# Optimization experiments

Measured on AMD Instinct MI355X. Metric: run time of the kernel, lower is better.

Reference implementation:

```python
import jax, jax.numpy as jnp
import numpy as np

B = 2048      # number of sequences with non-empty history
S = 32        # seq_len (all sequences full length for static shapes)
H = 256       # h_dim == embd_rank (ent/rel embedding dim)
NSEG = B * S  # total history timesteps (segments)
NNBR = 524288 # total gathered neighbor embeddings (avg 8 per segment)
ENT = 100000
REL = 1000


def setup_inputs() -> dict:
    key = jax.random.key(0)
    k1, k2, k3, k4, k5, k6, k7 = jax.random.split(key, 7)
    return {
        "neighbor_idx": jax.random.randint(k1, (NNBR,), 0, ENT),
        "segment_ids": jnp.sort(jax.random.randint(k2, (NNBR,), 0, NSEG)),
        "s_tem": jax.random.randint(k3, (B,), 0, ENT),
        "r_tem": jax.random.randint(k4, (B,), 0, REL),
        "s_hist_dt": jax.random.uniform(k5, (NSEG,), dtype=jnp.float32),
        "ent_embeds": jax.random.normal(k6, (ENT, H), dtype=jnp.float32),
        "rel_embeds": jax.random.normal(k7, (REL, H), dtype=jnp.float32),
    }


def reference(neighbor_idx, segment_ids, s_tem, r_tem, s_hist_dt, ent_embeds, rel_embeds):
    # gather neighbor entity embeddings (embeds_stack in the original)
    embeds_stack = ent_embeds[neighbor_idx]                     # [NNBR, H]
    # sparse.mm(mask, embeds_stack) == segment sum over neighbor groups
    sums = jax.ops.segment_sum(embeds_stack, segment_ids, num_segments=NSEG)
    counts = jax.ops.segment_sum(jnp.ones((NNBR,), embeds_stack.dtype),
                                 segment_ids, num_segments=NSEG)
    embeds_mean = sums / jnp.maximum(counts, 1.0)[:, None]      # [NSEG, H]
    # scatter means into padded [B, S, H] (all sequences full length)
    mean_seq = embeds_mean.reshape(B, S, H)
    # repeat subject entity / relation embeddings along time and concat
    ent_b = jnp.broadcast_to(ent_embeds[s_tem][:, None, :], (B, S, H))
    rel_b = jnp.broadcast_to(rel_embeds[r_tem][:, None, :], (B, S, H))
    s_embed_seq = jnp.concatenate([mean_seq, ent_b, rel_b], axis=-1)  # [B, S, 3H]
    s_hist_dt_seq = s_hist_dt.reshape(B, S)
    return s_embed_seq, s_hist_dt_seq
```

## Files before the change

kernel.cpp:

```cpp
#include <hip/hip_runtime.h>
#include <hip/hip_bf16.h>

#define BB    2048
#define SS    32
#define HH    256
#define NSEGC 65536
#define NNBRC 524288
#define NXCD  8
#define SPW   4

using f32x4 = __attribute__((ext_vector_type(4))) float;

__global__ __launch_bounds__(256) void seg_bounds_dt_kernel(
    const int*   __restrict__ segment_ids,
    int*         __restrict__ start,
    const float* __restrict__ dt,
    float*       __restrict__ out_tail)
{
    const int i = blockIdx.x * blockDim.x + threadIdx.x;

    if (i < NSEGC / 4) {
        const f32x4 v = reinterpret_cast<const f32x4*>(dt)[i];
        __builtin_nontemporal_store(v, reinterpret_cast<f32x4*>(out_tail) + i);
    }

    if (i > NSEGC) return;
    int lo = 0, hi = NNBRC;
    while (lo < hi) {
        const int mid = (lo + hi) >> 1;
        if (segment_ids[mid] < i) lo = mid + 1;
        else hi = mid;
    }
    start[i] = lo;
}

__global__ __launch_bounds__(256) void agg_kernel(
    const int*   __restrict__ neighbor_idx,
    const int*   __restrict__ s_tem,
    const int*   __restrict__ r_tem,
    const float* __restrict__ ent,
    const float* __restrict__ rel,
    const int*   __restrict__ start,
    float*       __restrict__ out)
{
    const int chunkw = gridDim.x / NXCD;
    const int wg   = (blockIdx.x % NXCD) * chunkw + blockIdx.x / NXCD;
    const int wave = wg * 4 + (threadIdx.x >> 6);
    const int lane = threadIdx.x & 63;
    const int seg0 = wave * SPW;
    const int b    = seg0 >> 5;

    const int sv = start[seg0 + min(lane, SPW)];
    const int p0 = __builtin_amdgcn_readfirstlane(__shfl(sv, 0));
    const int p1 = __builtin_amdgcn_readfirstlane(__shfl(sv, 1));
    const int p2 = __builtin_amdgcn_readfirstlane(__shfl(sv, 2));
    const int p3 = __builtin_amdgcn_readfirstlane(__shfl(sv, 3));
    const int p4 = __builtin_amdgcn_readfirstlane(__shfl(sv, 4));
    const int total = p4 - p0;
    const int r1 = p1 - p0, r2 = p2 - p0, r3 = p3 - p0;

    const int e = s_tem[b];
    const int r = r_tem[b];
    const f32x4 ev = *reinterpret_cast<const f32x4*>(ent + (size_t)e * HH + lane * 4);
    const f32x4 rv = *reinterpret_cast<const f32x4*>(rel + (size_t)r * HH + lane * 4);

    f32x4 a0 = {0.f,0.f,0.f,0.f}, a1 = a0, a2 = a0, a3 = a0;

    for (int base = 0; base < total; base += 64) {
        const int cnt = min(64, total - base);
        int myidx = 0;
        if (lane < cnt) myidx = neighbor_idx[p0 + base + lane];

        for (int j = 0; j < cnt; j += 8) {
            const int m = min(8, cnt - j);

#define GLD(K, VK)                                                         \
            f32x4 VK = {0.f,0.f,0.f,0.f};                                  \
            if (K < m) {                                                   \
                const int nb = __shfl(myidx, j + K);                       \
                VK = *reinterpret_cast<const f32x4*>(                      \
                    ent + (size_t)nb * HH + lane * 4);                     \
            }
            GLD(0, v0) GLD(1, v1) GLD(2, v2) GLD(3, v3)
            GLD(4, v4) GLD(5, v5) GLD(6, v6) GLD(7, v7)
#undef GLD

#define ACC(K, VK)                                                         \
            if (K < m) {                                                   \
                const int p = base + j + K;                                \
                if      (p < r1) a0 += VK;                                 \
                else if (p < r2) a1 += VK;                                 \
                else if (p < r3) a2 += VK;                                 \
                else             a3 += VK;                                 \
            }
            ACC(0, v0) ACC(1, v1) ACC(2, v2) ACC(3, v3)
            ACC(4, v4) ACC(5, v5) ACC(6, v6) ACC(7, v7)
#undef ACC
        }
    }

    const float i0 = 1.0f / fmaxf((float)(p1 - p0), 1.0f);
    const float i1 = 1.0f / fmaxf((float)(p2 - p1), 1.0f);
    const float i2 = 1.0f / fmaxf((float)(p3 - p2), 1.0f);
    const float i3 = 1.0f / fmaxf((float)(p4 - p3), 1.0f);

    float* o = out + (size_t)seg0 * (3 * HH);
#define STROW(S, AV, INV)                                                  \
    {                                                                      \
        const f32x4 mm = AV * INV;                                         \
        float* os = o + (size_t)(S) * (3 * HH);                            \
        __builtin_nontemporal_store(mm, reinterpret_cast<f32x4*>(os) + lane);          \
        __builtin_nontemporal_store(ev, reinterpret_cast<f32x4*>(os + HH) + lane);     \
        __builtin_nontemporal_store(rv, reinterpret_cast<f32x4*>(os + 2 * HH) + lane); \
    }
    STROW(0, a0, i0) STROW(1, a1, i1) STROW(2, a2, i2) STROW(3, a3, i3)
#undef STROW
}

extern "C" void kernel_launch(void* const* d_in, const int* in_sizes, int n_in,
                              void* d_out, int out_size, void* d_ws, size_t ws_size,
                              hipStream_t stream) {
    const int*   neighbor_idx = (const int*)  d_in[0];
    const int*   segment_ids  = (const int*)  d_in[1];
    const int*   s_tem        = (const int*)  d_in[2];
    const int*   r_tem        = (const int*)  d_in[3];
    const float* s_hist_dt    = (const float*)d_in[4];
    const float* ent_embeds   = (const float*)d_in[5];
    const float* rel_embeds   = (const float*)d_in[6];
    float*       out          = (float*)d_out;

    int* start = (int*)d_ws;

    {
        const int threads = 256;
        const int blocks  = (NSEGC + 1 + threads - 1) / threads;
        float* out_tail = out + (size_t)NSEGC * (3 * HH);
        seg_bounds_dt_kernel<<<blocks, threads, 0, stream>>>(
            segment_ids, start, s_hist_dt, out_tail);
    }

    {
        const int threads = 256;
        const int blocks  = NSEGC / SPW / 4;
        agg_kernel<<<blocks, threads, 0, stream>>>(
            neighbor_idx, s_tem, r_tem, ent_embeds, rel_embeds, start, out);
    }
}
```

Measured before the change: 336.6 us.

## Sweep entity-table chunks in order to localize neighbor gathers

Each wave now handles 8 segments (up to 192 neighbors per batch). For each batch it loops over 49 chunks of the entity table, using ballots to gather only the neighbors whose index falls in the current chunk. The idea is that all waves walk the table in roughly the same order at the same time, so the gathered rows hit L2/MALL more often. In exchange, each batch pays for 49 rounds of ballots, and the gathers become a serial one-row-at-a-time loop with little memory-level parallelism, where before 8 loads were issued together. Blocks grow to 512 threads.

```diff
diff --git a/kernel.cpp b/kernel.cpp
--- a/kernel.cpp
+++ b/kernel.cpp
@@ -7,7 +7,11 @@
 #define NSEGC 65536
 #define NNBRC 524288
 #define NXCD  8
-#define SPW   4
+#define SEGW  8
+#define WPB   8
+#define CHSH  11
+#define NCH   49
+#define SENT  0x7FFFFFFF
 
 using f32x4 = __attribute__((ext_vector_type(4))) float;
 
@@ -34,7 +38,7 @@
     start[i] = lo;
 }
 
-__global__ __launch_bounds__(256) void agg_kernel(
+__global__ __launch_bounds__(512, 4) void sweep_kernel(
     const int*   __restrict__ neighbor_idx,
     const int*   __restrict__ s_tem,
     const int*   __restrict__ r_tem,
@@ -45,75 +49,97 @@
 {
     const int chunkw = gridDim.x / NXCD;
     const int wg   = (blockIdx.x % NXCD) * chunkw + blockIdx.x / NXCD;
-    const int wave = wg * 4 + (threadIdx.x >> 6);
+    const int wave = wg * WPB + (threadIdx.x >> 6);
     const int lane = threadIdx.x & 63;
-    const int seg0 = wave * SPW;
+    const int seg0 = wave * SEGW;
     const int b    = seg0 >> 5;
 
-    const int sv = start[seg0 + min(lane, SPW)];
+    const int sv = start[seg0 + min(lane, SEGW)];
     const int p0 = __builtin_amdgcn_readfirstlane(__shfl(sv, 0));
-    const int p1 = __builtin_amdgcn_readfirstlane(__shfl(sv, 1));
-    const int p2 = __builtin_amdgcn_readfirstlane(__shfl(sv, 2));
-    const int p3 = __builtin_amdgcn_readfirstlane(__shfl(sv, 3));
-    const int p4 = __builtin_amdgcn_readfirstlane(__shfl(sv, 4));
-    const int total = p4 - p0;
-    const int r1 = p1 - p0, r2 = p2 - p0, r3 = p3 - p0;
+    const int q1 = __builtin_amdgcn_readfirstlane(__shfl(sv, 1));
+    const int q2 = __builtin_amdgcn_readfirstlane(__shfl(sv, 2));
+    const int q3 = __builtin_amdgcn_readfirstlane(__shfl(sv, 3));
+    const int q4 = __builtin_amdgcn_readfirstlane(__shfl(sv, 4));
+    const int q5 = __builtin_amdgcn_readfirstlane(__shfl(sv, 5));
+    const int q6 = __builtin_amdgcn_readfirstlane(__shfl(sv, 6));
+    const int q7 = __builtin_amdgcn_readfirstlane(__shfl(sv, 7));
+    const int q8 = __builtin_amdgcn_readfirstlane(__shfl(sv, 8));
+    const int total = q8 - p0;
+    const int r1 = q1-p0, r2 = q2-p0, r3 = q3-p0, r4 = q4-p0,
+              r5 = q5-p0, r6 = q6-p0, r7 = q7-p0;
+
+    f32x4 a0 = {0.f,0.f,0.f,0.f}, a1 = a0, a2 = a0, a3 = a0,
+          a4 = a0, a5 = a0, a6 = a0, a7 = a0;
+
+#define ACCUM(P, V)                                                        \
+    {                                                                      \
+        if ((P) < r4) {                                                    \
+            if ((P) < r2) { if ((P) < r1) a0 += (V); else a1 += (V); }     \
+            else          { if ((P) < r3) a2 += (V); else a3 += (V); }     \
+        } else {                                                           \
+            if ((P) < r6) { if ((P) < r5) a4 += (V); else a5 += (V); }     \
+            else          { if ((P) < r7) a6 += (V); else a7 += (V); }     \
+        }                                                                  \
+    }
+
+    for (int sb = 0; sb < total; sb += 192) {
+        const int scnt = min(192, total - sb);
+        int idx0 = SENT, idx1 = SENT, idx2 = SENT;
+        if (lane < scnt)       idx0 = neighbor_idx[p0 + sb + lane];
+        if (64 + lane < scnt)  idx1 = neighbor_idx[p0 + sb + 64 + lane];
+        if (128 + lane < scnt) idx2 = neighbor_idx[p0 + sb + 128 + lane];
+        const int ch0 = idx0 >> CHSH;
+        const int ch1 = idx1 >> CHSH;
+        const int ch2 = idx2 >> CHSH;
+
+        for (int c = 0; c < NCH; ++c) {
+            unsigned long long m0 = __ballot(ch0 == c);
+            unsigned long long m1 = __ballot(ch1 == c);
+            unsigned long long m2 = __ballot(ch2 == c);
+
+            while (m0) {
+                const int l = __builtin_ctzll(m0); m0 &= m0 - 1;
+                const int nb = __shfl(idx0, l);
+                const f32x4 v = *reinterpret_cast<const f32x4*>(
+                    ent + (size_t)nb * HH + lane * 4);
+                ACCUM(sb + l, v);
+            }
+            while (m1) {
+                const int l = __builtin_ctzll(m1); m1 &= m1 - 1;
+                const int nb = __shfl(idx1, l);
+                const f32x4 v = *reinterpret_cast<const f32x4*>(
+                    ent + (size_t)nb * HH + lane * 4);
+                ACCUM(sb + 64 + l, v);
+            }
+            while (m2) {
+                const int l = __builtin_ctzll(m2); m2 &= m2 - 1;
+                const int nb = __shfl(idx2, l);
+                const f32x4 v = *reinterpret_cast<const f32x4*>(
+                    ent + (size_t)nb * HH + lane * 4);
+                ACCUM(sb + 128 + l, v);
+            }
+        }
+    }
+#undef ACCUM
 
     const int e = s_tem[b];
     const int r = r_tem[b];
     const f32x4 ev = *reinterpret_cast<const f32x4*>(ent + (size_t)e * HH + lane * 4);
     const f32x4 rv = *reinterpret_cast<const f32x4*>(rel + (size_t)r * HH + lane * 4);
 
-    f32x4 a0 = {0.f,0.f,0.f,0.f}, a1 = a0, a2 = a0, a3 = a0;
-
-    for (int base = 0; base < total; base += 64) {
-        const int cnt = min(64, total - base);
-        int myidx = 0;
-        if (lane < cnt) myidx = neighbor_idx[p0 + base + lane];
-
-        for (int j = 0; j < cnt; j += 8) {
-            const int m = min(8, cnt - j);
-
-#define GLD(K, VK)                                                         \
-            f32x4 VK = {0.f,0.f,0.f,0.f};                                  \
-            if (K < m) {                                                   \
-                const int nb = __shfl(myidx, j + K);                       \
-                VK = *reinterpret_cast<const f32x4*>(                      \
-                    ent + (size_t)nb * HH + lane * 4);                     \
-            }
-            GLD(0, v0) GLD(1, v1) GLD(2, v2) GLD(3, v3)
-            GLD(4, v4) GLD(5, v5) GLD(6, v6) GLD(7, v7)
-#undef GLD
-
-#define ACC(K, VK)                                                         \
-            if (K < m) {                                                   \
-                const int p = base + j + K;                                \
-                if      (p < r1) a0 += VK;                                 \
-                else if (p < r2) a1 += VK;                                 \
-                else if (p < r3) a2 += VK;                                 \
-                else             a3 += VK;                                 \
-            }
-            ACC(0, v0) ACC(1, v1) ACC(2, v2) ACC(3, v3)
-            ACC(4, v4) ACC(5, v5) ACC(6, v6) ACC(7, v7)
-#undef ACC
-        }
-    }
-
-    const float i0 = 1.0f / fmaxf((float)(p1 - p0), 1.0f);
-    const float i1 = 1.0f / fmaxf((float)(p2 - p1), 1.0f);
-    const float i2 = 1.0f / fmaxf((float)(p3 - p2), 1.0f);
-    const float i3 = 1.0f / fmaxf((float)(p4 - p3), 1.0f);
-
     float* o = out + (size_t)seg0 * (3 * HH);
-#define STROW(S, AV, INV)                                                  \
+#define STROW(S, AV, CLO, CHI)                                             \
     {                                                                      \
-        const f32x4 mm = AV * INV;                                         \
+        const float inv = 1.0f / fmaxf((float)((CHI) - (CLO)), 1.0f);      \
+        const f32x4 mm = AV * inv;                                         \
         float* os = o + (size_t)(S) * (3 * HH);                            \
         __builtin_nontemporal_store(mm, reinterpret_cast<f32x4*>(os) + lane);          \
         __builtin_nontemporal_store(ev, reinterpret_cast<f32x4*>(os + HH) + lane);     \
         __builtin_nontemporal_store(rv, reinterpret_cast<f32x4*>(os + 2 * HH) + lane); \
     }
-    STROW(0, a0, i0) STROW(1, a1, i1) STROW(2, a2, i2) STROW(3, a3, i3)
+    STROW(0, a0, p0, q1) STROW(1, a1, q1, q2) STROW(2, a2, q2, q3)
+    STROW(3, a3, q3, q4) STROW(4, a4, q4, q5) STROW(5, a5, q5, q6)
+    STROW(6, a6, q6, q7) STROW(7, a7, q7, q8)
 #undef STROW
 }
 
@@ -140,9 +166,8 @@
     }
 
     {
-        const int threads = 256;
-        const int blocks  = NSEGC / SPW / 4;
-        agg_kernel<<<blocks, threads, 0, stream>>>(
+        const int blocks = NSEGC / (SEGW * WPB);
+        sweep_kernel<<<blocks, 512, 0, stream>>>(
             neighbor_idx, s_tem, r_tem, ent_embeds, rel_embeds, start, out);
     }
 }
```

After: 332.3 us. About the same (-1.3%).
